# Kernel tuning notes

Measured on AMD Instinct MI355X. Metric: run time of the kernel, lower is better.

The kernel has to match this reference:

```python
import jax, jax.numpy as jnp
import numpy as np

KS = 5
PAD = KS // 2
DIR = -1


def setup_inputs() -> dict:
    key = jax.random.key(0)
    k1, k2, k3 = jax.random.split(key, 3)
    B, C, H, W = 8, 64, 256, 256
    x = jax.random.normal(k1, (B, C, H, W), dtype=jnp.float32)
    # grouped 1x1 conv: groups=C, in-per-group=KS, out-per-group m=1 -> weight [C, 1, KS]
    weight = jax.random.normal(k2, (C, 1, KS), dtype=jnp.float32) * (1.0 / np.sqrt(KS))
    bias = jax.random.normal(k3, (C,), dtype=jnp.float32) * 0.01
    return {"x": x, "weight": weight, "bias": bias}


def _diag_dwconv(x, weight, bias):
    B, C, H, W = x.shape
    # im2col with kernel (1, KS), pad (0, PAD): tap i at (h, w) reads x[c, h, w + i - PAD]
    xp = jnp.pad(x, ((0, 0), (0, 0), (0, 0), (PAD, PAD)))
    taps = [xp[..., i:i + W] for i in range(KS)]  # each [B, C, H, W]
    # torch.roll with scalar shift and no dims rolls the FULLY FLATTENED tensor
    d_base = W  # W + 2*PAD - KS + 1 == W
    shifted = []
    for i in range(KS):
        t = taps[i]
        if i != PAD:
            shift = (i - PAD) * d_base if DIR == -1 else (PAD - i) * d_base
            t = jnp.roll(t.reshape(-1), shift).reshape(t.shape)
        shifted.append(t)
    cols = jnp.stack(shifted, axis=2)  # [B, C, KS, H, W] == view(B, C*KS, H, W)
    # grouped 1x1 conv, groups=C, m=1: out[b,c,m,h,w] = sum_k cols[b,c,k,h,w] * weight[c,m,k]
    out = jnp.einsum('bckhw,cmk->bcmhw', cols, weight)
    out = out.reshape(B, -1, H, W) + bias[None, :, None, None]
    return out


def reference(x, weight, bias):
    return _diag_dwconv(x, weight, bias)
```

## Files before the change

kernel.cpp:

```cpp
#include <hip/hip_runtime.h>


#define WIDTH 256
#define RTOT  131072
#define NTOT  (RTOT * WIDTH)
#define NCH   64
#define KS    5

__global__ __launch_bounds__(256) void diag_dwconv_kernel(
    const float* __restrict__ x,
    const float* __restrict__ wgt,
    const float* __restrict__ bias,
    float* __restrict__ out)
{
    int v  = blockIdx.x * blockDim.x + threadIdx.x;
    int r  = v >> 5;
    int w0 = (v & 31) << 3;
    int c  = (r >> 8) & (NCH - 1);

    float b = bias[c];
    float acc[8];
    #pragma unroll
    for (int j = 0; j < 8; ++j) acc[j] = b;

    #pragma unroll
    for (int k = 0; k < KS; ++k) {
        int rk = r + 2 - k;
        if (rk < 0)          rk += RTOT;
        else if (rk >= RTOT) rk -= RTOT;
        int base = rk * WIDTH + w0;

        int loff = base - 2;
        if (loff < 0) loff = 0;
        int roff = base + 8;
        if (roff > NTOT - 2) roff = NTOT - 2;

        float2 L  = *reinterpret_cast<const float2*>(x + loff);
        float4 M1 = *reinterpret_cast<const float4*>(x + base);
        float4 M2 = *reinterpret_cast<const float4*>(x + base + 4);
        float2 R  = *reinterpret_cast<const float2*>(x + roff);

        if (w0 == 0)         { L.x = 0.f; L.y = 0.f; }
        if (w0 == WIDTH - 8) { R.x = 0.f; R.y = 0.f; }

        float F[12] = { L.x, L.y,
                        M1.x, M1.y, M1.z, M1.w,
                        M2.x, M2.y, M2.z, M2.w,
                        R.x, R.y };

        float wk = wgt[c * KS + k];
        #pragma unroll
        for (int j = 0; j < 8; ++j)
            acc[j] = fmaf(wk, F[j + k], acc[j]);
    }

    int ob = r * WIDTH + w0;
    *reinterpret_cast<float4*>(out + ob)     = make_float4(acc[0], acc[1], acc[2], acc[3]);
    *reinterpret_cast<float4*>(out + ob + 4) = make_float4(acc[4], acc[5], acc[6], acc[7]);
}

extern "C" void kernel_launch(void* const* d_in, const int* in_sizes, int n_in,
                              void* d_out, int out_size, void* d_ws, size_t ws_size,
                              hipStream_t stream) {
    const float* x    = (const float*)d_in[0];
    const float* wgt  = (const float*)d_in[1];
    const float* bias = (const float*)d_in[2];
    float* out        = (float*)d_out;

    int threads = 256;
    int blocks  = (out_size / 8 + threads - 1) / threads;
    diag_dwconv_kernel<<<blocks, threads, 0, stream>>>(x, wgt, bias, out);
}
```

Measured before the change: 56.12 us.

## Compute four rows per thread to reuse loaded taps and use nontemporal stores

Measured after the change: 75.77 us. 1.35x slower.

```diff
diff --git a/kernel.cpp b/kernel.cpp
--- a/kernel.cpp
+++ b/kernel.cpp
@@ -7,6 +7,8 @@
 #define NCH   64
 #define KS    5
 
+typedef float f32x4 __attribute__((ext_vector_type(4)));
+
 __global__ __launch_bounds__(256) void diag_dwconv_kernel(
     const float* __restrict__ x,
     const float* __restrict__ wgt,
@@ -14,18 +16,27 @@
     float* __restrict__ out)
 {
     int v  = blockIdx.x * blockDim.x + threadIdx.x;
-    int r  = v >> 5;
+    int rq = (v >> 5) << 2;
     int w0 = (v & 31) << 3;
-    int c  = (r >> 8) & (NCH - 1);
+    int c  = (rq >> 8) & (NCH - 1);
 
+    float wv[KS];
+    #pragma unroll
+    for (int k = 0; k < KS; ++k) wv[k] = wgt[c * KS + k];
     float b = bias[c];
-    float acc[8];
+
+    float acc[4][8];
     #pragma unroll
-    for (int j = 0; j < 8; ++j) acc[j] = b;
+    for (int i = 0; i < 4; ++i)
+        #pragma unroll
+        for (int jj = 0; jj < 8; ++jj) acc[i][jj] = b;
+
+    bool edgeL = (w0 == 0);
+    bool edgeR = (w0 == WIDTH - 8);
 
     #pragma unroll
-    for (int k = 0; k < KS; ++k) {
-        int rk = r + 2 - k;
+    for (int j = -2; j <= 5; ++j) {
+        int rk = rq + j;
         if (rk < 0)          rk += RTOT;
         else if (rk >= RTOT) rk -= RTOT;
         int base = rk * WIDTH + w0;
@@ -40,23 +51,33 @@
         float4 M2 = *reinterpret_cast<const float4*>(x + base + 4);
         float2 R  = *reinterpret_cast<const float2*>(x + roff);
 
-        if (w0 == 0)         { L.x = 0.f; L.y = 0.f; }
-        if (w0 == WIDTH - 8) { R.x = 0.f; R.y = 0.f; }
+        if (edgeL) { L.x = 0.f; L.y = 0.f; }
+        if (edgeR) { R.x = 0.f; R.y = 0.f; }
 
         float F[12] = { L.x, L.y,
                         M1.x, M1.y, M1.z, M1.w,
                         M2.x, M2.y, M2.z, M2.w,
                         R.x, R.y };
 
-        float wk = wgt[c * KS + k];
         #pragma unroll
-        for (int j = 0; j < 8; ++j)
-            acc[j] = fmaf(wk, F[j + k], acc[j]);
+        for (int i = 0; i < 4; ++i) {
+            int k = i - j + 2;
+            if (k >= 0 && k < KS) {
+                #pragma unroll
+                for (int jj = 0; jj < 8; ++jj)
+                    acc[i][jj] = fmaf(wv[k], F[jj + k], acc[i][jj]);
+            }
+        }
     }
 
-    int ob = r * WIDTH + w0;
-    *reinterpret_cast<float4*>(out + ob)     = make_float4(acc[0], acc[1], acc[2], acc[3]);
-    *reinterpret_cast<float4*>(out + ob + 4) = make_float4(acc[4], acc[5], acc[6], acc[7]);
+    #pragma unroll
+    for (int i = 0; i < 4; ++i) {
+        int ob = (rq + i) * WIDTH + w0;
+        f32x4 lo = { acc[i][0], acc[i][1], acc[i][2], acc[i][3] };
+        f32x4 hi = { acc[i][4], acc[i][5], acc[i][6], acc[i][7] };
+        __builtin_nontemporal_store(lo, reinterpret_cast<f32x4*>(out + ob));
+        __builtin_nontemporal_store(hi, reinterpret_cast<f32x4*>(out + ob + 4));
+    }
 }
 
 extern "C" void kernel_launch(void* const* d_in, const int* in_sizes, int n_in,
@@ -68,6 +89,6 @@
     float* out        = (float*)d_out;
 
     int threads = 256;
-    int blocks  = (out_size / 8 + threads - 1) / threads;
+    int blocks  = (out_size / 32 + threads - 1) / threads;
     diag_dwconv_kernel<<<blocks, threads, 0, stream>>>(x, wgt, bias, out);
 }
```
